# Optimization experiments

Hardware: AMD Instinct MI355X
Metric: run time of the kernel (lower is better)

Reference implementation:

```python
import jax, jax.numpy as jnp
import numpy as np

S, B, H, I, E = 512, 2, 1024, 2816, 8  # seq_len, batch, hidden, intermediate, num_local_experts


def setup_inputs() -> dict:
    key = jax.random.key(0)
    ks = jax.random.split(key, 5)
    return {
        "hidden_states": jax.random.normal(ks[0], (S, B, H), dtype=jnp.float32),
        "router_w": jax.random.normal(ks[1], (E, H), dtype=jnp.float32) * 0.02,
        "gate_w": jax.random.normal(ks[2], (E, I, H), dtype=jnp.float32) * 0.02,
        "up_w": jax.random.normal(ks[3], (E, I, H), dtype=jnp.float32) * 0.02,
        "down_w": jax.random.normal(ks[4], (E, H, I), dtype=jnp.float32) * 0.02,
    }


def reference(hidden_states, router_w, gate_w, up_w, down_w):
    # Router: linear hidden -> num_experts, top-1 routing (num_experts_per_tok == 1).
    router_logits = jnp.einsum('sbh,eh->sbe', hidden_states, router_w)  # [S,B,E]
    routing_indices = jnp.argmax(router_logits, axis=-1)  # [S,B], top-1 == argmax
    # NOTE: the source computes routing_weights = sigmoid(top logit) but never
    # applies it in _combine_expert_outputs; we faithfully omit the scaling.

    out = jnp.zeros_like(hidden_states)
    for e in range(E):  # fixed small expert count; masked dense dispatch/combine
        mask = (routing_indices == e)[..., None]  # [S,B,1]
        xe = jnp.where(mask, hidden_states, 0.0)
        g = jnp.einsum('sbh,ih->sbi', xe, gate_w[e])
        u = jnp.einsum('sbh,ih->sbi', xe, up_w[e])
        ye = jnp.einsum('sbi,hi->sbh', jax.nn.silu(g) * u, down_w[e])
        out = out + jnp.where(mask, ye, 0.0)
    return out
```

## Files before the change

### kernel.cpp

```cpp
#include <hip/hip_runtime.h>
#include <math.h>

constexpr int H_ = 1024;
constexpr int I_ = 2816;
constexpr int E_ = 8;
constexpr int T_ = 1024;

typedef __bf16 bf16x8 __attribute__((ext_vector_type(8)));
typedef float f32x4 __attribute__((ext_vector_type(4)));

__device__ __forceinline__ ushort f2bf(float f) {
    uint32_t u = __float_as_uint(f);
    u += 0x7fff + ((u >> 16) & 1);
    return (ushort)(u >> 16);
}
__device__ __forceinline__ uint pack2(float lo, float hi) {
    return (uint)f2bf(lo) | ((uint)f2bf(hi) << 16);
}
__device__ __forceinline__ bf16x8 cvt8(float4 a, float4 b) {
    union { uint u[4]; bf16x8 v; } r;
    r.u[0] = pack2(a.x, a.y); r.u[1] = pack2(a.z, a.w);
    r.u[2] = pack2(b.x, b.y); r.u[3] = pack2(b.z, b.w);
    return r.v;
}

__device__ __forceinline__ void async_copy16(void* lds, const void* g) {
    __builtin_amdgcn_global_load_lds(
        (const __attribute__((address_space(1))) void*)g,
        (__attribute__((address_space(3))) void*)lds, 16, 0, 0);
}

__device__ __forceinline__ bf16x8 ldsA(const ushort* base, int row, int quad) {
    int bir = (quad * 16) ^ (((row >> 1) & 3) << 4);
    return *(const bf16x8*)((const char*)base + row * 64 + bir);
}
__device__ __forceinline__ bf16x8 ldsB(const float* base, int row, int quad) {
    int sw = (row & 7) << 4;
    const char* r = (const char*)base + row * 128;
    float4 x = *(const float4*)(r + ((quad * 32) ^ sw));
    float4 y = *(const float4*)(r + ((quad * 32 + 16) ^ sw));
    return cvt8(x, y);
}


__global__ __launch_bounds__(64) void router_kernel(const float* __restrict__ hidden,
                                                    const float* __restrict__ rw,
                                                    int* __restrict__ counts,
                                                    int* __restrict__ tlist,
                                                    ushort* __restrict__ xbf) {
    const int t = blockIdx.x;
    const int lane = threadIdx.x;
    const float* x = hidden + (size_t)t * H_ + lane * 16;
    float4 v[4];
#pragma unroll
    for (int j = 0; j < 4; j++) v[j] = ((const float4*)x)[j];
    uint2* xb = (uint2*)(xbf + (size_t)t * H_ + lane * 16);
#pragma unroll
    for (int j = 0; j < 4; j++) xb[j] = make_uint2(pack2(v[j].x, v[j].y), pack2(v[j].z, v[j].w));
    float acc[E_];
#pragma unroll
    for (int e = 0; e < E_; e++) {
        const float4* r = (const float4*)(rw + e * H_ + lane * 16);
        float a = 0.f;
#pragma unroll
        for (int j = 0; j < 4; j++) {
            float4 rv = r[j];
            a += v[j].x * rv.x + v[j].y * rv.y + v[j].z * rv.z + v[j].w * rv.w;
        }
        acc[e] = a;
    }
#pragma unroll
    for (int e = 0; e < E_; e++) {
#pragma unroll
        for (int off = 32; off >= 1; off >>= 1)
            acc[e] += __shfl_xor(acc[e], off, 64);
    }
    if (lane == 0) {
        int best = 0;
        float bv = acc[0];
#pragma unroll
        for (int e = 1; e < E_; e++) {
            if (acc[e] > bv) { bv = acc[e]; best = e; }
        }
        int pos = atomicAdd(&counts[best], 1);
        tlist[best * T_ + pos] = t;
    }
}

__global__ __launch_bounds__(256, 3) void gateup_kernel(const ushort* __restrict__ xbf,
                                                        const float* __restrict__ gate_w,
                                                        const float* __restrict__ up_w,
                                                        const int* __restrict__ counts,
                                                        const int* __restrict__ tlist,
                                                        ushort* __restrict__ act) {
    const int e  = blockIdx.y;
    const int i0 = blockIdx.x * 32;
    const int cnt = counts[e];
    const int tid = threadIdx.x;
    const int wv = tid >> 6, lane = tid & 63, quad = lane >> 4, l15 = lane & 15;

    __shared__ ushort Xs[2 * 256 * 32];
    __shared__ float  Gs[2 * 32 * 32];
    __shared__ float  Us[2 * 32 * 32];
    __shared__ int toks[256];

    const int wrow = tid >> 3;
    const int wbir = ((tid & 7) << 4) ^ ((wrow & 7) << 4);
    const float* gsrc = gate_w + ((size_t)e * I_ + i0 + wrow) * H_ + (wbir >> 2);
    const float* usrc = up_w   + ((size_t)e * I_ + i0 + wrow) * H_ + (wbir >> 2);

    for (int toff = 0; toff < cnt; toff += 256) {
        __syncthreads();
        { int p = toff + tid; toks[tid] = (p < cnt) ? tlist[e * T_ + p] : -1; }
        __syncthreads();

        const ushort* xsrc[4];
#pragma unroll
        for (int p = 0; p < 4; p++) {
            int row = p * 64 + (tid >> 2);
            int tok = toks[row];
            if (tok < 0) tok = 0;
            int birl = ((tid & 3) << 4) ^ (((row >> 1) & 3) << 4);
            xsrc[p] = xbf + (size_t)tok * H_ + (birl >> 1);
        }

        f32x4 accg[4][2], accu[4][2];
#pragma unroll
        for (int mi = 0; mi < 4; mi++)
#pragma unroll
            for (int nj = 0; nj < 2; nj++) {
                accg[mi][nj] = (f32x4){0.f, 0.f, 0.f, 0.f};
                accu[mi][nj] = (f32x4){0.f, 0.f, 0.f, 0.f};
            }

#define GSTAGE(buf, kofs) do {                                                  \
        char* xb_ = (char*)Xs + (buf) * 16384 + wv * 1024;                      \
        _Pragma("unroll")                                                       \
        for (int p = 0; p < 4; p++)                                             \
            async_copy16(xb_ + p * 4096, xsrc[p] + (kofs));                     \
        async_copy16((char*)Gs + (buf) * 4096 + wv * 1024, gsrc + (kofs));      \
        async_copy16((char*)Us + (buf) * 4096 + wv * 1024, usrc + (kofs));      \
    } while (0)

        GSTAGE(0, 0);
        int cur = 0;
#pragma unroll 1
        for (int k0 = 0; k0 < H_; k0 += 32) {
            if (k0 + 32 < H_) {
                GSTAGE(cur ^ 1, k0 + 32);
                asm volatile("s_waitcnt vmcnt(6)" ::: "memory");
            } else {
                asm volatile("s_waitcnt vmcnt(0)" ::: "memory");
            }
            __builtin_amdgcn_s_barrier();
            __builtin_amdgcn_sched_barrier(0);

            const ushort* Xb = Xs + cur * 8192;
            const float*  Gb = Gs + cur * 1024;
            const float*  Ub = Us + cur * 1024;
            bf16x8 a[4], bg[2], bu[2];
#pragma unroll
            for (int nj = 0; nj < 2; nj++) {
                bg[nj] = ldsB(Gb, nj * 16 + l15, quad);
                bu[nj] = ldsB(Ub, nj * 16 + l15, quad);
            }
#pragma unroll
            for (int mi = 0; mi < 4; mi++)
                a[mi] = ldsA(Xb, wv * 64 + mi * 16 + l15, quad);
#pragma unroll
            for (int mi = 0; mi < 4; mi++)
#pragma unroll
                for (int nj = 0; nj < 2; nj++) {
                    accg[mi][nj] = __builtin_amdgcn_mfma_f32_16x16x32_bf16(a[mi], bg[nj], accg[mi][nj], 0, 0, 0);
                    accu[mi][nj] = __builtin_amdgcn_mfma_f32_16x16x32_bf16(a[mi], bu[nj], accu[mi][nj], 0, 0, 0);
                }
            __builtin_amdgcn_sched_barrier(0);
            __builtin_amdgcn_s_barrier();
            __builtin_amdgcn_sched_barrier(0);
            cur ^= 1;
        }
#undef GSTAGE

#pragma unroll
        for (int mi = 0; mi < 4; mi++)
#pragma unroll
            for (int r = 0; r < 4; r++) {
                int tok = toks[wv * 64 + mi * 16 + quad * 4 + r];
                if (tok < 0) continue;
#pragma unroll
                for (int nj = 0; nj < 2; nj++) {
                    float g = accg[mi][nj][r], u = accu[mi][nj][r];
                    float s = g / (1.f + __expf(-g)) * u;
                    act[(size_t)tok * I_ + i0 + nj * 16 + l15] = f2bf(s);
                }
            }
    }
}

__global__ __launch_bounds__(256, 2) void down_kernel(const ushort* __restrict__ act,
                                                      const float* __restrict__ down_w,
                                                      const int* __restrict__ counts,
                                                      const int* __restrict__ tlist,
                                                      float* __restrict__ out) {
    const int e  = blockIdx.y;
    const int h0 = blockIdx.x * 16;
    const int cnt = counts[e];
    const int tid = threadIdx.x;
    const int wv = tid >> 6, lane = tid & 63, quad = lane >> 4, l15 = lane & 15;

    __shared__ ushort As[3 * 256 * 32];
    __shared__ float  Ds[3 * 16 * 32];
    __shared__ int toks[256];

    const int wrow = (tid >> 3) & 15;
    const int wbir = ((tid & 7) << 4) ^ ((wrow & 7) << 4);
    const float* dsrc = down_w + ((size_t)e * H_ + h0 + wrow) * I_ + (wbir >> 2);

    for (int toff = 0; toff < cnt; toff += 256) {
        __syncthreads();
        { int p = toff + tid; toks[tid] = (p < cnt) ? tlist[e * T_ + p] : -1; }
        __syncthreads();

        const ushort* asrc[4];
#pragma unroll
        for (int p = 0; p < 4; p++) {
            int row = p * 64 + (tid >> 2);
            int tok = toks[row];
            if (tok < 0) tok = 0;
            int birl = ((tid & 3) << 4) ^ (((row >> 1) & 3) << 4);
            asrc[p] = act + (size_t)tok * I_ + (birl >> 1);
        }

        f32x4 acc[4];
#pragma unroll
        for (int mi = 0; mi < 4; mi++) acc[mi] = (f32x4){0.f, 0.f, 0.f, 0.f};

#define DSTAGE(buf, kofs) do {                                                  \
        char* ab_ = (char*)As + (buf) * 16384 + wv * 1024;                      \
        _Pragma("unroll")                                                       \
        for (int p = 0; p < 4; p++)                                             \
            async_copy16(ab_ + p * 4096, asrc[p] + (kofs));                     \
        if (wv < 2)                                                             \
            async_copy16((char*)Ds + (buf) * 2048 + wv * 1024, dsrc + (kofs));  \
    } while (0)

        DSTAGE(0, 0);
        DSTAGE(1, 32);
        int cur = 0;
#pragma unroll 1
        for (int k0 = 0; k0 < I_; k0 += 32) {
            if (k0 + 64 < I_) {
                int stg = cur ? cur - 1 : 2;
                DSTAGE(stg, k0 + 64);
                if (wv < 2) asm volatile("s_waitcnt vmcnt(10)" ::: "memory");
                else        asm volatile("s_waitcnt vmcnt(8)"  ::: "memory");
            } else if (k0 + 32 < I_) {
                if (wv < 2) asm volatile("s_waitcnt vmcnt(5)" ::: "memory");
                else        asm volatile("s_waitcnt vmcnt(4)" ::: "memory");
            } else {
                asm volatile("s_waitcnt vmcnt(0)" ::: "memory");
            }
            __builtin_amdgcn_s_barrier();
            __builtin_amdgcn_sched_barrier(0);

            const ushort* Ab = As + cur * 8192;
            const float*  Db = Ds + cur * 512;
            bf16x8 a[4];
            bf16x8 bd = ldsB(Db, l15, quad);
#pragma unroll
            for (int mi = 0; mi < 4; mi++)
                a[mi] = ldsA(Ab, wv * 64 + mi * 16 + l15, quad);
#pragma unroll
            for (int mi = 0; mi < 4; mi++)
                acc[mi] = __builtin_amdgcn_mfma_f32_16x16x32_bf16(a[mi], bd, acc[mi], 0, 0, 0);

            __builtin_amdgcn_sched_barrier(0);
            __builtin_amdgcn_s_barrier();
            __builtin_amdgcn_sched_barrier(0);
            cur = (cur == 2) ? 0 : cur + 1;
        }
#undef DSTAGE

#pragma unroll
        for (int mi = 0; mi < 4; mi++)
#pragma unroll
            for (int r = 0; r < 4; r++) {
                int tok = toks[wv * 64 + mi * 16 + quad * 4 + r];
                if (tok < 0) continue;
                out[(size_t)tok * H_ + h0 + l15] = acc[mi][r];
            }
    }
}

extern "C" void kernel_launch(void* const* d_in, const int* in_sizes, int n_in,
                              void* d_out, int out_size, void* d_ws, size_t ws_size,
                              hipStream_t stream) {
    const float* hidden = (const float*)d_in[0];
    const float* rw     = (const float*)d_in[1];
    const float* gate_w = (const float*)d_in[2];
    const float* up_w   = (const float*)d_in[3];
    const float* down_w = (const float*)d_in[4];
    float* out = (float*)d_out;

    int* counts = (int*)d_ws;
    int* tlist  = counts + E_;
    ushort* xbf = (ushort*)(tlist + E_ * T_);
    ushort* act = xbf + (size_t)T_ * H_;

    hipMemsetAsync(counts, 0, E_ * sizeof(int), stream);
    hipLaunchKernelGGL(router_kernel, dim3(T_), dim3(64), 0, stream, hidden, rw, counts, tlist, xbf);
    hipLaunchKernelGGL(gateup_kernel, dim3(I_ / 32, E_), dim3(256), 0, stream,
                       xbf, gate_w, up_w, counts, tlist, act);
    hipLaunchKernelGGL(down_kernel, dim3(H_ / 16, E_), dim3(256), 0, stream,
                       act, down_w, counts, tlist, out);
}
```

Measured before the change: 382.9 us.

## Triple-buffer gate/up pipeline, single barrier per step, interleave experts, packed bf16 convert

The gate/up kernel moves from double to triple buffering with a prefetch distance of two stages. Both kernels now issue the next async stage after the barrier, which removes the second barrier per k-step. The grid is flattened with the expert index in the low bits, so blocks for different experts run side by side and load is balanced across CUs. The software float-to-bf16 rounding for weights is replaced by the hardware v_cvt_pk_bf16_f32 instruction, at the cost of more LDS and lower occupancy (launch bounds 3 to 2) in gate/up.

```diff
diff --git a/kernel.cpp b/kernel.cpp
--- a/kernel.cpp
+++ b/kernel.cpp
@@ -17,10 +17,12 @@
 __device__ __forceinline__ uint pack2(float lo, float hi) {
     return (uint)f2bf(lo) | ((uint)f2bf(hi) << 16);
 }
-__device__ __forceinline__ bf16x8 cvt8(float4 a, float4 b) {
+__device__ __forceinline__ bf16x8 cvt8pk(float4 a, float4 b) {
     union { uint u[4]; bf16x8 v; } r;
-    r.u[0] = pack2(a.x, a.y); r.u[1] = pack2(a.z, a.w);
-    r.u[2] = pack2(b.x, b.y); r.u[3] = pack2(b.z, b.w);
+    asm("v_cvt_pk_bf16_f32 %0, %1, %2" : "=v"(r.u[0]) : "v"(a.x), "v"(a.y));
+    asm("v_cvt_pk_bf16_f32 %0, %1, %2" : "=v"(r.u[1]) : "v"(a.z), "v"(a.w));
+    asm("v_cvt_pk_bf16_f32 %0, %1, %2" : "=v"(r.u[2]) : "v"(b.x), "v"(b.y));
+    asm("v_cvt_pk_bf16_f32 %0, %1, %2" : "=v"(r.u[3]) : "v"(b.z), "v"(b.w));
     return r.v;
 }
 
@@ -28,18 +30,6 @@
     __builtin_amdgcn_global_load_lds(
         (const __attribute__((address_space(1))) void*)g,
         (__attribute__((address_space(3))) void*)lds, 16, 0, 0);
-}
-
-__device__ __forceinline__ bf16x8 ldsA(const ushort* base, int row, int quad) {
-    int bir = (quad * 16) ^ (((row >> 1) & 3) << 4);
-    return *(const bf16x8*)((const char*)base + row * 64 + bir);
-}
-__device__ __forceinline__ bf16x8 ldsB(const float* base, int row, int quad) {
-    int sw = (row & 7) << 4;
-    const char* r = (const char*)base + row * 128;
-    float4 x = *(const float4*)(r + ((quad * 32) ^ sw));
-    float4 y = *(const float4*)(r + ((quad * 32 + 16) ^ sw));
-    return cvt8(x, y);
 }
 
 
@@ -87,41 +77,44 @@
     }
 }
 
-__global__ __launch_bounds__(256, 3) void gateup_kernel(const ushort* __restrict__ xbf,
+__global__ __launch_bounds__(256, 2) void gateup_kernel(const ushort* __restrict__ xbf,
                                                         const float* __restrict__ gate_w,
                                                         const float* __restrict__ up_w,
                                                         const int* __restrict__ counts,
                                                         const int* __restrict__ tlist,
                                                         ushort* __restrict__ act) {
-    const int e  = blockIdx.y;
-    const int i0 = blockIdx.x * 32;
+    const int id = blockIdx.x;
+    const int e  = id & 7;
+    const int i0 = (id >> 3) * 32;
     const int cnt = counts[e];
     const int tid = threadIdx.x;
     const int wv = tid >> 6, lane = tid & 63, quad = lane >> 4, l15 = lane & 15;
 
-    __shared__ ushort Xs[2 * 256 * 32];
-    __shared__ float  Gs[2 * 32 * 32];
-    __shared__ float  Us[2 * 32 * 32];
+    __shared__ ushort Xs[3 * 8192];
+    __shared__ float  Gs[3 * 1024];
+    __shared__ float  Us[3 * 1024];
     __shared__ int toks[256];
 
-    const int wrow = tid >> 3;
-    const int wbir = ((tid & 7) << 4) ^ ((wrow & 7) << 4);
-    const float* gsrc = gate_w + ((size_t)e * I_ + i0 + wrow) * H_ + (wbir >> 2);
-    const float* usrc = up_w   + ((size_t)e * I_ + i0 + wrow) * H_ + (wbir >> 2);
+    const int rg = wv * 8 + (lane >> 3);
+    const int cg = ((lane & 7) ^ (rg & 7)) << 2;
+    const float* gsp = gate_w + ((size_t)e * I_ + i0 + rg) * H_ + cg;
+    const float* usp = up_w   + ((size_t)e * I_ + i0 + rg) * H_ + cg;
+    const int wdstF = wv * 256 + lane * 4;
 
     for (int toff = 0; toff < cnt; toff += 256) {
         __syncthreads();
         { int p = toff + tid; toks[tid] = (p < cnt) ? tlist[e * T_ + p] : -1; }
         __syncthreads();
 
-        const ushort* xsrc[4];
+        const ushort* xsp[4];
+        int xdst[4];
 #pragma unroll
         for (int p = 0; p < 4; p++) {
-            int row = p * 64 + (tid >> 2);
-            int tok = toks[row];
-            if (tok < 0) tok = 0;
-            int birl = ((tid & 3) << 4) ^ (((row >> 1) & 3) << 4);
-            xsrc[p] = xbf + (size_t)tok * H_ + (birl >> 1);
+            int rp = wv * 64 + p * 16 + (lane >> 2);
+            int tok = toks[rp]; if (tok < 0) tok = 0;
+            int q = (lane & 3) ^ ((rp >> 1) & 3);
+            xsp[p] = xbf + (size_t)tok * H_ + q * 8;
+            xdst[p] = wv * 2048 + p * 512 + lane * 8;
         }
 
         f32x4 accg[4][2], accu[4][2];
@@ -133,40 +126,45 @@
                 accu[mi][nj] = (f32x4){0.f, 0.f, 0.f, 0.f};
             }
 
-#define GSTAGE(buf, kofs) do {                                                  \
-        char* xb_ = (char*)Xs + (buf) * 16384 + wv * 1024;                      \
+#define GSTAGE(b, k) do {                                                       \
         _Pragma("unroll")                                                       \
         for (int p = 0; p < 4; p++)                                             \
-            async_copy16(xb_ + p * 4096, xsrc[p] + (kofs));                     \
-        async_copy16((char*)Gs + (buf) * 4096 + wv * 1024, gsrc + (kofs));      \
-        async_copy16((char*)Us + (buf) * 4096 + wv * 1024, usrc + (kofs));      \
+            async_copy16(&Xs[(b) * 8192 + xdst[p]], xsp[p] + (k));              \
+        async_copy16(&Gs[(b) * 1024 + wdstF], gsp + (k));                       \
+        async_copy16(&Us[(b) * 1024 + wdstF], usp + (k));                       \
     } while (0)
 
         GSTAGE(0, 0);
-        int cur = 0;
+        GSTAGE(1, 32);
+        int cur = 0, sb = 2;
 #pragma unroll 1
-        for (int k0 = 0; k0 < H_; k0 += 32) {
-            if (k0 + 32 < H_) {
-                GSTAGE(cur ^ 1, k0 + 32);
-                asm volatile("s_waitcnt vmcnt(6)" ::: "memory");
-            } else {
-                asm volatile("s_waitcnt vmcnt(0)" ::: "memory");
-            }
+        for (int t = 0; t < 32; ++t) {
+            if (t < 31) asm volatile("s_waitcnt vmcnt(6)" ::: "memory");
+            else        asm volatile("s_waitcnt vmcnt(0)" ::: "memory");
+            __builtin_amdgcn_sched_barrier(0);
             __builtin_amdgcn_s_barrier();
             __builtin_amdgcn_sched_barrier(0);
-
-            const ushort* Xb = Xs + cur * 8192;
-            const float*  Gb = Gs + cur * 1024;
-            const float*  Ub = Us + cur * 1024;
+            if (t < 30) { GSTAGE(sb, t * 32 + 64); __builtin_amdgcn_sched_barrier(0); }
+
+            const ushort* Xb = &Xs[cur * 8192];
+            const float*  Gb = &Gs[cur * 1024];
+            const float*  Ub = &Us[cur * 1024];
             bf16x8 a[4], bg[2], bu[2];
 #pragma unroll
             for (int nj = 0; nj < 2; nj++) {
-                bg[nj] = ldsB(Gb, nj * 16 + l15, quad);
-                bu[nj] = ldsB(Ub, nj * 16 + l15, quad);
-            }
-#pragma unroll
-            for (int mi = 0; mi < 4; mi++)
-                a[mi] = ldsA(Xb, wv * 64 + mi * 16 + l15, quad);
+                int rr = nj * 16 + l15;
+                int c0 = (2 * quad) ^ (rr & 7), c1 = (2 * quad + 1) ^ (rr & 7);
+                bg[nj] = cvt8pk(*(const float4*)(Gb + rr * 32 + c0 * 4),
+                                *(const float4*)(Gb + rr * 32 + c1 * 4));
+                bu[nj] = cvt8pk(*(const float4*)(Ub + rr * 32 + c0 * 4),
+                                *(const float4*)(Ub + rr * 32 + c1 * 4));
+            }
+#pragma unroll
+            for (int mi = 0; mi < 4; mi++) {
+                int r = wv * 64 + mi * 16 + l15;
+                int qq = quad ^ ((r >> 1) & 3);
+                a[mi] = *(const bf16x8*)(Xb + r * 32 + qq * 8);
+            }
 #pragma unroll
             for (int mi = 0; mi < 4; mi++)
 #pragma unroll
@@ -175,9 +173,8 @@
                     accu[mi][nj] = __builtin_amdgcn_mfma_f32_16x16x32_bf16(a[mi], bu[nj], accu[mi][nj], 0, 0, 0);
                 }
             __builtin_amdgcn_sched_barrier(0);
-            __builtin_amdgcn_s_barrier();
-            __builtin_amdgcn_sched_barrier(0);
-            cur ^= 1;
+            cur = (cur == 2) ? 0 : cur + 1;
+            sb  = (sb  == 2) ? 0 : sb  + 1;
         }
 #undef GSTAGE
 
@@ -202,82 +199,87 @@
                                                       const int* __restrict__ counts,
                                                       const int* __restrict__ tlist,
                                                       float* __restrict__ out) {
-    const int e  = blockIdx.y;
-    const int h0 = blockIdx.x * 16;
+    const int id = blockIdx.x;
+    const int e  = id & 7;
+    const int h0 = (id >> 3) * 16;
     const int cnt = counts[e];
     const int tid = threadIdx.x;
     const int wv = tid >> 6, lane = tid & 63, quad = lane >> 4, l15 = lane & 15;
 
-    __shared__ ushort As[3 * 256 * 32];
-    __shared__ float  Ds[3 * 16 * 32];
+    __shared__ ushort As[3 * 8192];
+    __shared__ float  Ws[3 * 512];
     __shared__ int toks[256];
 
-    const int wrow = (tid >> 3) & 15;
-    const int wbir = ((tid & 7) << 4) ^ ((wrow & 7) << 4);
-    const float* dsrc = down_w + ((size_t)e * H_ + h0 + wrow) * I_ + (wbir >> 2);
+    const int rw_ = (wv & 1) * 8 + (lane >> 3);
+    const int cw  = ((lane & 7) ^ (rw_ & 7)) << 2;
+    const float* wsp = down_w + ((size_t)e * H_ + h0 + rw_) * I_ + cw;
+    const int ddstF = (wv & 1) * 256 + lane * 4;
 
     for (int toff = 0; toff < cnt; toff += 256) {
         __syncthreads();
         { int p = toff + tid; toks[tid] = (p < cnt) ? tlist[e * T_ + p] : -1; }
         __syncthreads();
 
-        const ushort* asrc[4];
+        const ushort* asp[4];
+        int adst[4];
 #pragma unroll
         for (int p = 0; p < 4; p++) {
-            int row = p * 64 + (tid >> 2);
-            int tok = toks[row];
-            if (tok < 0) tok = 0;
-            int birl = ((tid & 3) << 4) ^ (((row >> 1) & 3) << 4);
-            asrc[p] = act + (size_t)tok * I_ + (birl >> 1);
+            int rp = wv * 64 + p * 16 + (lane >> 2);
+            int tok = toks[rp]; if (tok < 0) tok = 0;
+            int q = (lane & 3) ^ ((rp >> 1) & 3);
+            asp[p] = act + (size_t)tok * I_ + q * 8;
+            adst[p] = wv * 2048 + p * 512 + lane * 8;
         }
 
         f32x4 acc[4];
 #pragma unroll
         for (int mi = 0; mi < 4; mi++) acc[mi] = (f32x4){0.f, 0.f, 0.f, 0.f};
 
-#define DSTAGE(buf, kofs) do {                                                  \
-        char* ab_ = (char*)As + (buf) * 16384 + wv * 1024;                      \
+#define DSTAGE(b, k) do {                                                       \
         _Pragma("unroll")                                                       \
         for (int p = 0; p < 4; p++)                                             \
-            async_copy16(ab_ + p * 4096, asrc[p] + (kofs));                     \
+            async_copy16(&As[(b) * 8192 + adst[p]], asp[p] + (k));              \
         if (wv < 2)                                                             \
-            async_copy16((char*)Ds + (buf) * 2048 + wv * 1024, dsrc + (kofs));  \
+            async_copy16(&Ws[(b) * 512 + ddstF], wsp + (k));                    \
     } while (0)
 
         DSTAGE(0, 0);
         DSTAGE(1, 32);
-        int cur = 0;
+        int cur = 0, sb = 2;
 #pragma unroll 1
-        for (int k0 = 0; k0 < I_; k0 += 32) {
-            if (k0 + 64 < I_) {
-                int stg = cur ? cur - 1 : 2;
-                DSTAGE(stg, k0 + 64);
-                if (wv < 2) asm volatile("s_waitcnt vmcnt(10)" ::: "memory");
-                else        asm volatile("s_waitcnt vmcnt(8)"  ::: "memory");
-            } else if (k0 + 32 < I_) {
+        for (int t = 0; t < 88; ++t) {
+            if (t < 87) {
                 if (wv < 2) asm volatile("s_waitcnt vmcnt(5)" ::: "memory");
                 else        asm volatile("s_waitcnt vmcnt(4)" ::: "memory");
             } else {
                 asm volatile("s_waitcnt vmcnt(0)" ::: "memory");
             }
+            __builtin_amdgcn_sched_barrier(0);
             __builtin_amdgcn_s_barrier();
             __builtin_amdgcn_sched_barrier(0);
-
-            const ushort* Ab = As + cur * 8192;
-            const float*  Db = Ds + cur * 512;
+            if (t < 86) { DSTAGE(sb, t * 32 + 64); __builtin_amdgcn_sched_barrier(0); }
+
+            const ushort* Ab = &As[cur * 8192];
+            const float*  Wb = &Ws[cur * 512];
             bf16x8 a[4];
-            bf16x8 bd = ldsB(Db, l15, quad);
-#pragma unroll
-            for (int mi = 0; mi < 4; mi++)
-                a[mi] = ldsA(Ab, wv * 64 + mi * 16 + l15, quad);
-#pragma unroll
-            for (int mi = 0; mi < 4; mi++)
-                acc[mi] = __builtin_amdgcn_mfma_f32_16x16x32_bf16(a[mi], bd, acc[mi], 0, 0, 0);
-
-            __builtin_amdgcn_sched_barrier(0);
-            __builtin_amdgcn_s_barrier();
+            {
+                int rr = l15;
+                int c0 = (2 * quad) ^ (rr & 7), c1 = (2 * quad + 1) ^ (rr & 7);
+                bf16x8 bd = cvt8pk(*(const float4*)(Wb + rr * 32 + c0 * 4),
+                                   *(const float4*)(Wb + rr * 32 + c1 * 4));
+#pragma unroll
+                for (int mi = 0; mi < 4; mi++) {
+                    int r = wv * 64 + mi * 16 + l15;
+                    int qq = quad ^ ((r >> 1) & 3);
+                    a[mi] = *(const bf16x8*)(Ab + r * 32 + qq * 8);
+                }
+#pragma unroll
+                for (int mi = 0; mi < 4; mi++)
+                    acc[mi] = __builtin_amdgcn_mfma_f32_16x16x32_bf16(a[mi], bd, acc[mi], 0, 0, 0);
+            }
             __builtin_amdgcn_sched_barrier(0);
             cur = (cur == 2) ? 0 : cur + 1;
+            sb  = (sb  == 2) ? 0 : sb  + 1;
         }
 #undef DSTAGE
 
@@ -309,8 +311,8 @@
 
     hipMemsetAsync(counts, 0, E_ * sizeof(int), stream);
     hipLaunchKernelGGL(router_kernel, dim3(T_), dim3(64), 0, stream, hidden, rw, counts, tlist, xbf);
-    hipLaunchKernelGGL(gateup_kernel, dim3(I_ / 32, E_), dim3(256), 0, stream,
+    hipLaunchKernelGGL(gateup_kernel, dim3((I_ / 32) * E_), dim3(256), 0, stream,
                        xbf, gate_w, up_w, counts, tlist, act);
-    hipLaunchKernelGGL(down_kernel, dim3(H_ / 16, E_), dim3(256), 0, stream,
+    hipLaunchKernelGGL(down_kernel, dim3((H_ / 16) * E_), dim3(256), 0, stream,
                        act, down_w, counts, tlist, out);
 }
```

Result: no change. 389.5 us (+1.7%).
